# Kernel tuning notes

Measured on AMD Instinct MI355X. Metric: run time of the kernel, lower is better.

Reference implementation:

```python
import jax, jax.numpy as jnp
import numpy as np

N, E, G = 50000, 1600000, 500
H, F, NG, L, OUT = 128, 128, 50, 6, 1
LOG2 = float(np.log(2.0))

def ssp(x):
    return jax.nn.softplus(x) - LOG2

def setup_inputs() -> dict:
    key = jax.random.key(0)
    ks = jax.random.split(key, 16)
    inp = {
        'z': jax.random.randint(ks[0], (N,), 0, 100),
        'pos': jax.random.normal(ks[1], (N, 3), jnp.float32) * 5.0,
        'batch': jnp.sort(jax.random.randint(ks[2], (N,), 0, G)),
        'edge_index': jax.random.randint(ks[3], (2, E), 0, N),
        # parameters
        'emb': jax.random.normal(ks[4], (100, H), jnp.float32) * 0.1,
        'dist_W': jax.random.normal(ks[5], (1, NG), jnp.float32) * 0.1,
        'dist_b': jnp.zeros((NG,), jnp.float32),
        'Wn': jax.random.normal(ks[6], (L, H, F), jnp.float32) * (1.0 / np.sqrt(H)),
        'We': jax.random.normal(ks[7], (L, NG, F), jnp.float32) * (1.0 / np.sqrt(NG)),
        'be': jnp.zeros((L, F), jnp.float32),
        'Wo': jax.random.normal(ks[8], (L, F, H), jnp.float32) * (1.0 / np.sqrt(F)),
        'bo': jnp.zeros((L, H), jnp.float32),
        'W1': jax.random.normal(ks[9], (H, H // 2), jnp.float32) * (1.0 / np.sqrt(H)),
        'b1': jnp.zeros((H // 2,), jnp.float32),
        'W2': jax.random.normal(ks[10], (H // 2, OUT), jnp.float32) * (1.0 / np.sqrt(H // 2)),
        'b2': jnp.zeros((OUT,), jnp.float32),
    }
    return inp

def reference(z, pos, batch, edge_index, emb, dist_W, dist_b, Wn, We, be, Wo, bo, W1, b1, W2, b2):
    row, col = edge_index[0], edge_index[1]
    # edge distances -> Linear(1, num_gaussians)
    dist = jnp.linalg.norm(pos[row] - pos[col], axis=-1)            # [E]
    e = dist[:, None] * dist_W[0][None, :] + dist_b                 # [E, NG]
    v = emb[z]                                                      # [N, H]
    # edge-conditioned message passing x num_layers
    for i in range(Wn.shape[0]):
        h = v @ Wn[i]                                               # [N, F]
        msg = h[col] * (e @ We[i] + be[i])                          # [E, F]
        agg = jax.ops.segment_sum(msg, row, num_segments=v.shape[0])
        v = ssp(agg @ Wo[i] + bo[i])                                # [N, H]
    # readout
    u = ssp(v @ W1 + b1) @ W2 + b2                                  # [N, OUT]
    return jax.ops.segment_sum(u, batch, num_segments=G)            # [G, OUT]
```

## Files before the change

### kernel.cpp

```cpp
#include <hip/hip_runtime.h>
#include <math.h>

#define HDIM 128
#define NGAUSS 50
#define NLAYER 6
#define TSTR 136
#define DINV (1.0f/512.0f)
#define NXCD 8
#define NSTRIPE 512

typedef unsigned short ushortT;
typedef __attribute__((ext_vector_type(8))) short bf16x8;
typedef __attribute__((ext_vector_type(4))) float f32x4;

static __device__ __forceinline__ float bf2f(unsigned short u){
  union { unsigned int i; float f; } x; x.i = ((unsigned int)u) << 16; return x.f;
}
static __device__ __forceinline__ float bitsf(unsigned int i){
  union { unsigned int i; float f; } x; x.i = i; return x.f;
}
static __device__ __forceinline__ unsigned short f2bf(float f){
  union { float f; unsigned int i; } x; x.f = f;
  unsigned int i = x.i;
  unsigned int r = (i + 0x7FFFu + ((i >> 16) & 1u)) >> 16;
  return (unsigned short)r;
}
static __device__ __forceinline__ float ssp(float x){
  return fmaxf(x, 0.0f) + __logf(1.0f + __expf(-fabsf(x))) - 0.69314718055994530942f;
}
static __device__ __forceinline__ f32x4 mfma4r(const bf16x8* a, const bf16x8* b){
  f32x4 d = {0.f, 0.f, 0.f, 0.f};
  d = __builtin_amdgcn_mfma_f32_16x16x32_bf16(a[0], b[0], d, 0, 0, 0);
  d = __builtin_amdgcn_mfma_f32_16x16x32_bf16(a[1], b[1], d, 0, 0, 0);
  d = __builtin_amdgcn_mfma_f32_16x16x32_bf16(a[2], b[2], d, 0, 0, 0);
  d = __builtin_amdgcn_mfma_f32_16x16x32_bf16(a[3], b[3], d, 0, 0, 0);
  return d;
}


__global__ __launch_bounds__(256)
void k_colscan(int* __restrict__ hist, int* __restrict__ colTotal, int NB){
  __shared__ int sA[512], sB[512];
  int b = blockIdx.x, tid = threadIdx.x;
  sA[tid]       = hist[tid * 512 + b];
  sA[tid + 256] = hist[(tid + 256) * 512 + b];
  __syncthreads();
  int* pa = sA; int* pb = sB;
  for (int off = 1; off < 512; off <<= 1){
    for (int i = tid; i < 512; i += 256)
      pb[i] = pa[i] + (i >= off ? pa[i - off] : 0);
    __syncthreads();
    int* t = pa; pa = pb; pb = t;
  }
  int e0 = (tid == 0) ? 0 : pa[tid - 1];
  int e1 = pa[tid + 255];
  hist[tid * 512 + b]       = e0;
  hist[(tid + 256) * 512 + b] = e1;
  if (tid == 0) colTotal[b] = pa[511];
}

__global__ __launch_bounds__(256)
void k_bscan(const int* __restrict__ colTotal, int* __restrict__ bucketBase, int NB){
  __shared__ int sA[512], sB[512];
  int tid = threadIdx.x;
  for (int i = tid; i < 512; i += 256) sA[i] = (i < NB) ? colTotal[i] : 0;
  __syncthreads();
  int* pa = sA; int* pb = sB;
  for (int off = 1; off < 512; off <<= 1){
    for (int i = tid; i < 512; i += 256)
      pb[i] = pa[i] + (i >= off ? pa[i - off] : 0);
    __syncthreads();
    int* t = pa; pa = pb; pb = t;
  }
  for (int i = tid; i < NB; i += 256)
    bucketBase[i] = (i == 0) ? 0 : pa[i - 1];
  if (tid == 0) bucketBase[NB] = pa[NB - 1];
}

__global__ __launch_bounds__(256)
void k_scatter(const int* __restrict__ erow, const int* __restrict__ ecol,
               const float* __restrict__ pos, const int* __restrict__ hist,
               const int* __restrict__ bucketBase, uint2* __restrict__ stg,
               int E, int NB, int shift, int estripe){
  __shared__ int cur[512];
  int tid = threadIdx.x, w = blockIdx.x;
  for (int b = tid; b < NB; b += 256)
    cur[b] = bucketBase[b] + hist[w * 512 + b];
  __syncthreads();
  int beg = w * estripe;
  int end = beg + estripe; if (end > E) end = E;
  int mask = (1 << shift) - 1;
  for (int e = beg + tid; e < end; e += 256){
    int r = erow[e], c = ecol[e];
    float dx = pos[r*3+0] - pos[c*3+0];
    float dy = pos[r*3+1] - pos[c*3+1];
    float dz = pos[r*3+2] - pos[c*3+2];
    float d = sqrtf(dx*dx + dy*dy + dz*dz);
    int du = (int)(d * 512.0f + 0.5f);
    if (du > 65535) du = 65535;
    int p = atomicAdd(&cur[r >> shift], 1);
    uint2 t;
    t.x = ((unsigned int)c << 16) | (unsigned int)du;
    t.y = (unsigned int)(r & mask);
    stg[p] = t;
  }
}

__global__ __launch_bounds__(256)
void k_place(const uint2* __restrict__ stg, const int* __restrict__ bucketBase,
             int* __restrict__ offsets, unsigned int* __restrict__ csr,
             int N, int NB, int shift, int E){
  __shared__ int rc[1024];
  __shared__ int sA[1024], sB[1024];
  int b = blockIdx.x, tid = threadIdx.x;
  int R = 1 << shift;
  int r0 = b << shift;
  int s = bucketBase[b], e2 = bucketBase[b + 1];
  for (int i = tid; i < R; i += 256) rc[i] = 0;
  __syncthreads();
  for (int j = s + tid; j < e2; j += 256)
    atomicAdd(&rc[stg[j].y], 1);
  __syncthreads();
  for (int i = tid; i < R; i += 256) sA[i] = rc[i];
  __syncthreads();
  int* pa = sA; int* pb = sB;
  for (int off = 1; off < R; off <<= 1){
    for (int i = tid; i < R; i += 256)
      pb[i] = pa[i] + (i >= off ? pa[i - off] : 0);
    __syncthreads();
    int* t = pa; pa = pb; pb = t;
  }
  for (int i = tid; i < R; i += 256){
    int excl = (i == 0) ? 0 : pa[i - 1];
    rc[i] = excl;
    int r = r0 + i;
    if (r < N) offsets[r] = s + excl;
  }
  if (b == NB - 1 && tid == 0) offsets[N] = E;
  __syncthreads();
  for (int j = s + tid; j < e2; j += 256){
    uint2 t = stg[j];
    int slot = s + atomicAdd(&rc[t.y], 1);
    csr[slot] = t.x;
  }
}

__global__ __launch_bounds__(256)
void k_emb2(const float* __restrict__ emb, const float* __restrict__ Wn,
            ushortT* __restrict__ emb2){
  int idx = blockIdx.x * 256 + threadIdx.x;
  if (idx >= 100 * HDIM) return;
  int i = idx >> 7, f = idx & 127;
  float acc = 0.f;
  #pragma unroll 8
  for (int k = 0; k < HDIM; ++k)
    acc = fmaf(emb[i * HDIM + k], Wn[k * HDIM + f], acc);
  emb2[idx] = f2bf(acc);
}

__global__ void k_setup(const int* __restrict__ z, const ushortT* __restrict__ emb2,
                        ushortT* __restrict__ h0,
                        const float* __restrict__ Wn, ushortT* __restrict__ WnT,
                        const float* __restrict__ Wo, ushortT* __restrict__ WoT,
                        const float* __restrict__ dW, const float* __restrict__ db,
                        const float* __restrict__ We, const float* __restrict__ be,
                        float* __restrict__ a, float* __restrict__ c,
                        const int* __restrict__ batch, int* __restrict__ groupOff,
                        const float* __restrict__ W1, ushortT* __restrict__ W1T,
                        const int* __restrict__ erow, int* __restrict__ hist,
                        int N, int G, int E, int estripe, int NB, int shift,
                        int B1, int B2, int B4, int B5, int B7){
  __shared__ int lh[512];
  int b = blockIdx.x;
  int tid = threadIdx.x;
  if (b < B1){
    int base = (b * 256 + tid) * 8;
    if (base < N * HDIM){
      int n = base >> 7, f = base & 127;
      bf16x8 v = *(const bf16x8*)(emb2 + z[n] * HDIM + f);
      *(bf16x8*)(h0 + base) = v;
    }
    return;
  }
  b -= B1;
  if (b < B2){
    int base = (b * 256 + tid) * 8;
    if (base < NLAYER * HDIM * HDIM){
      int mat = base >> 14, rem = base & 16383;
      int n = rem >> 7, k0 = rem & 127;
      bf16x8 v;
      #pragma unroll
      for (int j = 0; j < 8; ++j)
        v[j] = (short)f2bf(Wn[(mat << 14) + (k0 + j) * HDIM + n]);
      *(bf16x8*)(WnT + base) = v;
    }
    return;
  }
  b -= B2;
  if (b < B2){
    int base = (b * 256 + tid) * 8;
    if (base < NLAYER * HDIM * HDIM){
      int mat = base >> 14, rem = base & 16383;
      int n = rem >> 7, k0 = rem & 127;
      bf16x8 v;
      #pragma unroll
      for (int j = 0; j < 8; ++j)
        v[j] = (short)f2bf(Wo[(mat << 14) + (k0 + j) * HDIM + n]);
      *(bf16x8*)(WoT + base) = v;
    }
    return;
  }
  b -= B2;
  if (b < B4){
    int idx = b * 256 + tid;
    if (idx < NLAYER * HDIM){
      int l = idx >> 7, f = idx & 127;
      float av = 0.f, cv = 0.f;
      for (int g = 0; g < NGAUSS; ++g){
        float we = We[(l * NGAUSS + g) * HDIM + f];
        av += dW[g] * we;
        cv += db[g] * we;
      }
      a[idx] = av;
      c[idx] = cv + be[idx];
    }
    return;
  }
  b -= B4;
  if (b < B5){
    int i = b * 256 + tid;
    if (i >= N) return;
    int bb = batch[i];
    if (i == 0){
      for (int g = 0; g <= bb; ++g) groupOff[g] = 0;
    } else {
      int pb = batch[i - 1];
      for (int g = pb + 1; g <= bb; ++g) groupOff[g] = i;
    }
    if (i == N - 1){
      for (int g = bb + 1; g <= G; ++g) groupOff[g] = N;
    }
    return;
  }
  b -= B5;
  if (b < B7){
    int base = (b * 256 + tid) * 8;
    if (base < 64 * HDIM){
      int ncol = base >> 7, k0 = base & 127;
      bf16x8 v;
      #pragma unroll
      for (int j = 0; j < 8; ++j)
        v[j] = (short)f2bf(W1[(k0 + j) * 64 + ncol]);
      *(bf16x8*)(W1T + base) = v;
    }
    return;
  }
  b -= B7;
  if (b < NSTRIPE){
    for (int i = tid; i < NB; i += 256) lh[i] = 0;
    __syncthreads();
    int beg = b * estripe;
    int end = beg + estripe; if (end > E) end = E;
    for (int e = beg + tid; e < end; e += 256)
      atomicAdd(&lh[erow[e] >> shift], 1);
    __syncthreads();
    for (int i = tid; i < NB; i += 256) hist[b * 512 + i] = lh[i];
  }
}

#define AGG_PROC(P, DD) do { \
    unsigned int w_; float lo_, hi_; \
    w_ = (P).x; lo_ = bitsf(w_ << 16); hi_ = bitsf(w_ & 0xFFFF0000u); \
    s1[0] = fmaf(lo_, (DD), s1[0]); s0[0] += lo_; \
    s1[1] = fmaf(hi_, (DD), s1[1]); s0[1] += hi_; \
    w_ = (P).y; lo_ = bitsf(w_ << 16); hi_ = bitsf(w_ & 0xFFFF0000u); \
    s1[2] = fmaf(lo_, (DD), s1[2]); s0[2] += lo_; \
    s1[3] = fmaf(hi_, (DD), s1[3]); s0[3] += hi_; \
    w_ = (P).z; lo_ = bitsf(w_ << 16); hi_ = bitsf(w_ & 0xFFFF0000u); \
    s1[4] = fmaf(lo_, (DD), s1[4]); s0[4] += lo_; \
    s1[5] = fmaf(hi_, (DD), s1[5]); s0[5] += hi_; \
    w_ = (P).w; lo_ = bitsf(w_ << 16); hi_ = bitsf(w_ & 0xFFFF0000u); \
    s1[6] = fmaf(lo_, (DD), s1[6]); s0[6] += lo_; \
    s1[7] = fmaf(hi_, (DD), s1[7]); s0[7] += hi_; \
  } while(0)

#define GATH(Q) (*(const uint4*)(h + ((size_t)((Q) >> 16) << 7) + fl))

__global__ __launch_bounds__(256, 6)
void k_agg2(const ushortT* __restrict__ h, const int* __restrict__ offsets,
            const unsigned int* __restrict__ cd, const float* __restrict__ a,
            const float* __restrict__ c, ushortT* __restrict__ aggHi,
            int N, int segNodes){
  int xcd = blockIdx.x & (NXCD - 1);
  int idx = blockIdx.x >> 3;
  int node = xcd * segNodes + idx * 4 + (threadIdx.x >> 6);
  if (node >= N || node >= (xcd + 1) * segNodes) return;
  int lane = threadIdx.x & 63;
  int quarter = lane >> 4;
  int fl = (lane & 15) * 8;
  int s = offsets[node], e = offsets[node + 1];
  float s0[8] = {0.f,0.f,0.f,0.f,0.f,0.f,0.f,0.f};
  float s1[8] = {0.f,0.f,0.f,0.f,0.f,0.f,0.f,0.f};
  int efull = s + ((e - s) & ~7);
  int L = s;
  if (efull - s >= 16){
    unsigned int qA0 = cd[L + quarter],      qA1 = cd[L + 4 + quarter];
    uint4 pA0 = GATH(qA0), pA1 = GATH(qA1);
    unsigned int qB0 = cd[L + 8 + quarter],  qB1 = cd[L + 12 + quarter];
    uint4 pB0 = GATH(qB0), pB1 = GATH(qB1);
    float dA0 = (float)(qA0 & 0xFFFFu) * DINV, dA1 = (float)(qA1 & 0xFFFFu) * DINV;
    float dB0 = (float)(qB0 & 0xFFFFu) * DINV, dB1 = (float)(qB1 & 0xFFFFu) * DINV;
    L += 16;
    for (; L + 16 <= efull; L += 16){
      unsigned int nA0 = cd[L + quarter], nA1 = cd[L + 4 + quarter];
      AGG_PROC(pA0, dA0); AGG_PROC(pA1, dA1);
      pA0 = GATH(nA0); pA1 = GATH(nA1);
      dA0 = (float)(nA0 & 0xFFFFu) * DINV; dA1 = (float)(nA1 & 0xFFFFu) * DINV;
      unsigned int nB0 = cd[L + 8 + quarter], nB1 = cd[L + 12 + quarter];
      AGG_PROC(pB0, dB0); AGG_PROC(pB1, dB1);
      pB0 = GATH(nB0); pB1 = GATH(nB1);
      dB0 = (float)(nB0 & 0xFFFFu) * DINV; dB1 = (float)(nB1 & 0xFFFFu) * DINV;
    }
    AGG_PROC(pA0, dA0); AGG_PROC(pA1, dA1);
    AGG_PROC(pB0, dB0); AGG_PROC(pB1, dB1);
  }
  for (; L + 8 <= efull; L += 8){
    unsigned int q0 = cd[L + quarter], q1 = cd[L + 4 + quarter];
    uint4 p0 = GATH(q0), p1 = GATH(q1);
    float d0 = (float)(q0 & 0xFFFFu) * DINV, d1 = (float)(q1 & 0xFFFFu) * DINV;
    AGG_PROC(p0, d0); AGG_PROC(p1, d1);
  }
  for (int j = efull; j < e; j += 4){
    int myj = j + quarter;
    if (myj < e){
      unsigned int q = cd[myj];
      uint4 p = GATH(q);
      float dd = (float)(q & 0xFFFFu) * DINV;
      AGG_PROC(p, dd);
    }
  }
  float4 av0 = *(const float4*)(a + fl);
  float4 av1 = *(const float4*)(a + fl + 4);
  float4 cv0 = *(const float4*)(c + fl);
  float4 cv1 = *(const float4*)(c + fl + 4);
  float r[8];
  r[0] = av0.x * s1[0] + cv0.x * s0[0];
  r[1] = av0.y * s1[1] + cv0.y * s0[1];
  r[2] = av0.z * s1[2] + cv0.z * s0[2];
  r[3] = av0.w * s1[3] + cv0.w * s0[3];
  r[4] = av1.x * s1[4] + cv1.x * s0[4];
  r[5] = av1.y * s1[5] + cv1.y * s0[5];
  r[6] = av1.z * s1[6] + cv1.z * s0[6];
  r[7] = av1.w * s1[7] + cv1.w * s0[7];
  #pragma unroll
  for (int k = 0; k < 8; ++k){
    r[k] += __shfl_down(r[k], 32, 64);
    r[k] += __shfl_down(r[k], 16, 64);
  }
  if (quarter == 0){
    uint4 st;
    st.x = (unsigned int)f2bf(r[0]) | ((unsigned int)f2bf(r[1]) << 16);
    st.y = (unsigned int)f2bf(r[2]) | ((unsigned int)f2bf(r[3]) << 16);
    st.z = (unsigned int)f2bf(r[4]) | ((unsigned int)f2bf(r[5]) << 16);
    st.w = (unsigned int)f2bf(r[6]) | ((unsigned int)f2bf(r[7]) << 16);
    *(uint4*)(aggHi + ((size_t)node << 7) + fl) = st;
  }
}

__global__ __launch_bounds__(256, 2)
void k_fpair(const ushortT* __restrict__ agg, const ushortT* __restrict__ WoT,
             const float* __restrict__ bo, const ushortT* __restrict__ WnT,
             ushortT* __restrict__ outH, int N, int segTiles){
  __shared__ ushortT vt[2][32 * TSTR];
  int tid = threadIdx.x;
  int wave = tid >> 6, lane = tid & 63;
  int pairI = wave >> 1, half = wave & 1;
  int m = lane & 15, quad = lane >> 4;
  int ntiles = (N + 15) >> 4;
  int xcd = blockIdx.x & (NXCD - 1);
  int idx = blockIdx.x >> 3;
  int wjIdx = idx * 2 + pairI;
  int segWJ = segTiles >> 1;
  int t0 = xcd * segTiles + wjIdx * 2;
  bool act = (wjIdx < segWJ) && (t0 < ntiles);
  ushortT* vw = vt[pairI];

  bf16x8 av[2][4];
  if (act){
    #pragma unroll
    for (int rt = 0; rt < 2; ++rt){
      int row = (t0 + rt) * 16 + m; if (row >= N) row = N - 1;
      #pragma unroll
      for (int kk = 0; kk < 4; ++kk)
        av[rt][kk] = *(const bf16x8*)(agg + ((size_t)row << 7) + kk*32 + quad*8);
    }
    #pragma unroll
    for (int cti = 0; cti < 4; ++cti){
      int ncol = (half * 4 + cti) * 16 + m;
      const ushortT* bp = WoT + ((size_t)ncol << 7) + quad*8;
      bf16x8 bb[4];
      #pragma unroll
      for (int kk = 0; kk < 4; ++kk) bb[kk] = *(const bf16x8*)(bp + kk*32);
      float bbias = bo[ncol];
      #pragma unroll
      for (int rt = 0; rt < 2; ++rt){
        f32x4 d = mfma4r(av[rt], bb);
        #pragma unroll
        for (int r = 0; r < 4; ++r)
          vw[(rt*16 + quad*4 + r) * TSTR + ncol] = f2bf(ssp(d[r] + bbias));
      }
    }
  }
  __syncthreads();
  if (act){
    bf16x8 a2[2][4];
    #pragma unroll
    for (int rt = 0; rt < 2; ++rt){
      #pragma unroll
      for (int kk = 0; kk < 4; ++kk)
        a2[rt][kk] = *(const bf16x8*)(&vw[(rt*16 + m) * TSTR + kk*32 + quad*8]);
    }
    #pragma unroll
    for (int cti = 0; cti < 4; ++cti){
      int ncol = (half * 4 + cti) * 16 + m;
      const ushortT* bp = WnT + ((size_t)ncol << 7) + quad*8;
      bf16x8 bb[4];
      #pragma unroll
      for (int kk = 0; kk < 4; ++kk) bb[kk] = *(const bf16x8*)(bp + kk*32);
      #pragma unroll
      for (int rt = 0; rt < 2; ++rt){
        f32x4 d = mfma4r(a2[rt], bb);
        #pragma unroll
        for (int r = 0; r < 4; ++r){
          int orow = (t0 + rt) * 16 + quad*4 + r;
          if (orow < N) outH[((size_t)orow << 7) + ncol] = f2bf(d[r]);
        }
      }
    }
  }
}

__global__ __launch_bounds__(256, 2)
void k_gfinal(const ushortT* __restrict__ agg, const ushortT* __restrict__ WoT,
              const float* __restrict__ bo, const ushortT* __restrict__ W1T,
              const float* __restrict__ b1, const float* __restrict__ W2,
              const float* __restrict__ b2, float* __restrict__ u,
              int N, int segTiles){
  __shared__ ushortT vt[2][32 * TSTR];
  __shared__ float part[2][2][32];
  int tid = threadIdx.x;
  int wave = tid >> 6, lane = tid & 63;
  int pairI = wave >> 1, half = wave & 1;
  int m = lane & 15, quad = lane >> 4;
  int ntiles = (N + 15) >> 4;
  int xcd = blockIdx.x & (NXCD - 1);
  int idx = blockIdx.x >> 3;
  int wjIdx = idx * 2 + pairI;
  int segWJ = segTiles >> 1;
  int t0 = xcd * segTiles + wjIdx * 2;
  bool act = (wjIdx < segWJ) && (t0 < ntiles);
  ushortT* vw = vt[pairI];

  if (act){
    bf16x8 av[2][4];
    #pragma unroll
    for (int rt = 0; rt < 2; ++rt){
      int row = (t0 + rt) * 16 + m; if (row >= N) row = N - 1;
      #pragma unroll
      for (int kk = 0; kk < 4; ++kk)
        av[rt][kk] = *(const bf16x8*)(agg + ((size_t)row << 7) + kk*32 + quad*8);
    }
    #pragma unroll
    for (int cti = 0; cti < 4; ++cti){
      int ncol = (half * 4 + cti) * 16 + m;
      const ushortT* bp = WoT + ((size_t)ncol << 7) + quad*8;
      bf16x8 bb[4];
      #pragma unroll
      for (int kk = 0; kk < 4; ++kk) bb[kk] = *(const bf16x8*)(bp + kk*32);
      float bbias = bo[ncol];
      #pragma unroll
      for (int rt = 0; rt < 2; ++rt){
        f32x4 d = mfma4r(av[rt], bb);
        #pragma unroll
        for (int r = 0; r < 4; ++r)
          vw[(rt*16 + quad*4 + r) * TSTR + ncol] = f2bf(ssp(d[r] + bbias));
      }
    }
  }
  __syncthreads();
  if (act){
    bf16x8 a2[2][4];
    #pragma unroll
    for (int rt = 0; rt < 2; ++rt){
      #pragma unroll
      for (int kk = 0; kk < 4; ++kk)
        a2[rt][kk] = *(const bf16x8*)(&vw[(rt*16 + m) * TSTR + kk*32 + quad*8]);
    }
    float acc[2][4] = {{0.f,0.f,0.f,0.f},{0.f,0.f,0.f,0.f}};
    #pragma unroll
    for (int cti = 0; cti < 2; ++cti){
      int ncol = (half * 2 + cti) * 16 + m;
      const ushortT* bp = W1T + ((size_t)ncol << 7) + quad*8;
      bf16x8 bb[4];
      #pragma unroll
      for (int kk = 0; kk < 4; ++kk) bb[kk] = *(const bf16x8*)(bp + kk*32);
      float bb1 = b1[ncol];
      float w2  = W2[ncol];
      #pragma unroll
      for (int rt = 0; rt < 2; ++rt){
        f32x4 d = mfma4r(a2[rt], bb);
        #pragma unroll
        for (int r = 0; r < 4; ++r)
          acc[rt][r] += ssp(d[r] + bb1) * w2;
      }
    }
    #pragma unroll
    for (int rt = 0; rt < 2; ++rt){
      #pragma unroll
      for (int r = 0; r < 4; ++r){
        float v = acc[rt][r];
        v += __shfl_xor(v, 1, 64);
        v += __shfl_xor(v, 2, 64);
        v += __shfl_xor(v, 4, 64);
        v += __shfl_xor(v, 8, 64);
        if (m == 0) part[pairI][half][rt*16 + quad*4 + r] = v;
      }
    }
  }
  __syncthreads();
  if (tid < 64){
    int p = tid >> 5, row = tid & 31;
    int wj = idx * 2 + p;
    int tt = xcd * segTiles + wj * 2;
    if (wj < segWJ && tt < ntiles){
      int orow = tt * 16 + row;
      if (orow < N) u[orow] = part[p][0][row] + part[p][1][row] + b2[0];
    }
  }
}

__global__ void k_gsum(const float* __restrict__ u, const int* __restrict__ groupOff,
                       float* __restrict__ out, int G){
  int g = blockIdx.x * 4 + (threadIdx.x >> 6);
  if (g >= G) return;
  int lane = threadIdx.x & 63;
  int s = groupOff[g], e = groupOff[g + 1];
  float acc = 0.f;
  for (int j = s + lane; j < e; j += 64) acc += u[j];
  #pragma unroll
  for (int off = 32; off > 0; off >>= 1)
    acc += __shfl_down(acc, off, 64);
  if (lane == 0) out[g] = acc;
}

extern "C" void kernel_launch(void* const* d_in, const int* in_sizes, int n_in,
                              void* d_out, int out_size, void* d_ws, size_t ws_size,
                              hipStream_t stream){
  const int N = in_sizes[0];
  const int E = in_sizes[3] / 2;
  const int G = out_size;

  const int*   z     = (const int*)d_in[0];
  const float* pos   = (const float*)d_in[1];
  const int*   batch = (const int*)d_in[2];
  const int*   eidx  = (const int*)d_in[3];
  const int*   erow  = eidx;
  const int*   ecol  = eidx + E;
  const float* emb   = (const float*)d_in[4];
  const float* dW    = (const float*)d_in[5];
  const float* db    = (const float*)d_in[6];
  const float* Wn    = (const float*)d_in[7];
  const float* We    = (const float*)d_in[8];
  const float* be    = (const float*)d_in[9];
  const float* Wo    = (const float*)d_in[10];
  const float* bo    = (const float*)d_in[11];
  const float* W1    = (const float*)d_in[12];
  const float* b1    = (const float*)d_in[13];
  const float* W2    = (const float*)d_in[14];
  const float* b2    = (const float*)d_in[15];

  char* ws = (char*)d_ws;
  size_t off = 0;
  auto alloc = [&](size_t bytes) -> char* {
    char* p = ws + off;
    off = (off + bytes + 255) & ~(size_t)255;
    return p;
  };
  size_t hbytes = (size_t)N * HDIM * 2;
  size_t stgbytes = (size_t)E * 8;
  int*          offsets  = (int*)         alloc((size_t)(N + 1) * 4);
  unsigned int* csr      = (unsigned int*)alloc((size_t)E * 4);
  ushortT*      h0       = (ushortT*)     alloc(hbytes);
  ushortT*      h1       = (ushortT*)     alloc(hbytes);
  ushortT*      agghi    = (ushortT*)     alloc(hbytes);
  ushortT*      stgbuf   = (ushortT*)     alloc(stgbytes);
  ushortT*      emb2     = (ushortT*)     alloc((size_t)100 * HDIM * 2);
  ushortT*      WnT      = (ushortT*)     alloc((size_t)NLAYER * HDIM * HDIM * 2);
  ushortT*      WoT      = (ushortT*)     alloc((size_t)NLAYER * HDIM * HDIM * 2);
  ushortT*      W1T      = (ushortT*)     alloc((size_t)64 * HDIM * 2);
  float*        a        = (float*)       alloc((size_t)NLAYER * HDIM * 4);
  float*        c        = (float*)       alloc((size_t)NLAYER * HDIM * 4);
  float*        u        = (float*)       alloc((size_t)N * 4);
  int*          groupOff = (int*)         alloc((size_t)(G + 1) * 4);

  int*   hist       = (int*)h1;
  int*   colTotal   = hist + NSTRIPE * 512;
  int*   bucketBase = colTotal + 512;
  uint2* stg        = (uint2*)stgbuf;

  int shift = 7;
  while ((((N - 1) >> shift) + 1) > 512) ++shift;
  int NB = ((N - 1) >> shift) + 1;
  int estripe = (E + NSTRIPE - 1) / NSTRIPE;

  int B1 = (N * HDIM / 8 + 255) / 256;
  int B2 = (NLAYER * HDIM * HDIM / 8 + 255) / 256;
  int B4 = (NLAYER * HDIM + 255) / 256;
  int B5 = (N + 255) / 256;
  int B7 = (64 * HDIM / 8 + 255) / 256;

  k_emb2<<<(100 * HDIM + 255) / 256, 256, 0, stream>>>(emb, Wn, emb2);
  k_setup<<<B1 + 2*B2 + B4 + B5 + B7 + NSTRIPE, 256, 0, stream>>>(
      z, emb2, h0, Wn, WnT, Wo, WoT,
      dW, db, We, be, a, c, batch, groupOff, W1, W1T,
      erow, hist,
      N, G, E, estripe, NB, shift, B1, B2, B4, B5, B7);

  k_colscan<<<NB,      256, 0, stream>>>(hist, colTotal, NB);
  k_bscan  <<<1,       256, 0, stream>>>(colTotal, bucketBase, NB);
  k_scatter<<<NSTRIPE, 256, 0, stream>>>(erow, ecol, pos, hist, bucketBase,
                                         stg, E, NB, shift, estripe);
  k_place  <<<NB,      256, 0, stream>>>(stg, bucketBase, offsets, csr, N, NB, shift, E);

  int ntiles = (N + 15) >> 4;
  int segTiles = (((ntiles + NXCD - 1) / NXCD) + 1) & ~1;
  int segNodes = segTiles * 16;
  int segWJ = segTiles >> 1;
  int aggGrid  = NXCD * ((segNodes + 3) / 4);
  int gGrid    = NXCD * ((segWJ + 1) / 2);

  for (int l = 0; l < NLAYER; ++l){
    size_t wo = (size_t)l * HDIM * HDIM;
    const ushortT* hin  = (l & 1) ? h1 : h0;
    ushortT*       hout = (l & 1) ? h0 : h1;
    k_agg2<<<aggGrid, 256, 0, stream>>>(hin, offsets, csr,
                                        a + l * HDIM, c + l * HDIM, agghi, N, segNodes);
    if (l < NLAYER - 1){
      size_t wn = (size_t)(l + 1) * HDIM * HDIM;
      k_fpair<<<gGrid, 256, 0, stream>>>(agghi, WoT + wo, bo + (size_t)l * HDIM,
                                         WnT + wn, hout, N, segTiles);
    } else {
      k_gfinal<<<gGrid, 256, 0, stream>>>(agghi, WoT + wo, bo + (size_t)l * HDIM,
                                          W1T, b1, W2, b2, u, N, segTiles);
    }
  }
  k_gsum<<<(G + 3) / 4, 256, 0, stream>>>(u, groupOff, (float*)d_out, G);
}
```

Before: 567.2 us.

## Fold small setup kernels into neighbours to cut launch count

Merges the embedding projection into the setup kernel and moves the h0 gather into the column-scan launch. The single-block bucket scan is dropped, and each scatter and place block recomputes the 512-entry scan itself. The group-sum kernel is replaced by atomic adds from the final readout kernel into an output that setup zeroes. This removes three kernel launches and the serialization they cause. In exchange each block does redundant scan work and there are float atomics on output, so summation order is no longer deterministic.

```diff
diff --git a/kernel.cpp b/kernel.cpp
--- a/kernel.cpp
+++ b/kernel.cpp
@@ -39,9 +39,19 @@
 
 
 __global__ __launch_bounds__(256)
-void k_colscan(int* __restrict__ hist, int* __restrict__ colTotal, int NB){
+void k_colscan(int* __restrict__ hist, int* __restrict__ colTotal,
+               const int* __restrict__ z, const ushortT* __restrict__ emb2,
+               ushortT* __restrict__ h0, int N, int NB){
   __shared__ int sA[512], sB[512];
   int b = blockIdx.x, tid = threadIdx.x;
+  if (b >= NB){
+    int base = ((b - NB) * 256 + tid) * 8;
+    if (base < N * HDIM){
+      int n = base >> 7, f = base & 127;
+      *(bf16x8*)(h0 + base) = *(const bf16x8*)(emb2 + z[n] * HDIM + f);
+    }
+    return;
+  }
   sA[tid]       = hist[tid * 512 + b];
   sA[tid + 256] = hist[(tid + 256) * 512 + b];
   __syncthreads();
@@ -60,9 +70,13 @@
 }
 
 __global__ __launch_bounds__(256)
-void k_bscan(const int* __restrict__ colTotal, int* __restrict__ bucketBase, int NB){
+void k_scatter(const int* __restrict__ erow, const int* __restrict__ ecol,
+               const float* __restrict__ pos, const int* __restrict__ hist,
+               const int* __restrict__ colTotal, uint2* __restrict__ stg,
+               int E, int NB, int shift, int estripe){
+  __shared__ int cur[512];
   __shared__ int sA[512], sB[512];
-  int tid = threadIdx.x;
+  int tid = threadIdx.x, w = blockIdx.x;
   for (int i = tid; i < 512; i += 256) sA[i] = (i < NB) ? colTotal[i] : 0;
   __syncthreads();
   int* pa = sA; int* pb = sB;
@@ -72,20 +86,8 @@
     __syncthreads();
     int* t = pa; pa = pb; pb = t;
   }
-  for (int i = tid; i < NB; i += 256)
-    bucketBase[i] = (i == 0) ? 0 : pa[i - 1];
-  if (tid == 0) bucketBase[NB] = pa[NB - 1];
-}
-
-__global__ __launch_bounds__(256)
-void k_scatter(const int* __restrict__ erow, const int* __restrict__ ecol,
-               const float* __restrict__ pos, const int* __restrict__ hist,
-               const int* __restrict__ bucketBase, uint2* __restrict__ stg,
-               int E, int NB, int shift, int estripe){
-  __shared__ int cur[512];
-  int tid = threadIdx.x, w = blockIdx.x;
   for (int b = tid; b < NB; b += 256)
-    cur[b] = bucketBase[b] + hist[w * 512 + b];
+    cur[b] = ((b == 0) ? 0 : pa[b - 1]) + hist[w * 512 + b];
   __syncthreads();
   int beg = w * estripe;
   int end = beg + estripe; if (end > E) end = E;
@@ -107,7 +109,7 @@
 }
 
 __global__ __launch_bounds__(256)
-void k_place(const uint2* __restrict__ stg, const int* __restrict__ bucketBase,
+void k_place(const uint2* __restrict__ stg, const int* __restrict__ colTotal,
              int* __restrict__ offsets, unsigned int* __restrict__ csr,
              int N, int NB, int shift, int E){
   __shared__ int rc[1024];
@@ -115,7 +117,18 @@
   int b = blockIdx.x, tid = threadIdx.x;
   int R = 1 << shift;
   int r0 = b << shift;
-  int s = bucketBase[b], e2 = bucketBase[b + 1];
+  for (int i = tid; i < 512; i += 256) sA[i] = (i < NB) ? colTotal[i] : 0;
+  __syncthreads();
+  int* pa = sA; int* pb = sB;
+  for (int off = 1; off < 512; off <<= 1){
+    for (int i = tid; i < 512; i += 256)
+      pb[i] = pa[i] + (i >= off ? pa[i - off] : 0);
+    __syncthreads();
+    int* t = pa; pa = pb; pb = t;
+  }
+  int s  = (b == 0) ? 0 : pa[b - 1];
+  int e2 = pa[b];
+  __syncthreads();
   for (int i = tid; i < R; i += 256) rc[i] = 0;
   __syncthreads();
   for (int j = s + tid; j < e2; j += 256)
@@ -123,7 +136,7 @@
   __syncthreads();
   for (int i = tid; i < R; i += 256) sA[i] = rc[i];
   __syncthreads();
-  int* pa = sA; int* pb = sB;
+  pa = sA; pb = sB;
   for (int off = 1; off < R; off <<= 1){
     for (int i = tid; i < R; i += 256)
       pb[i] = pa[i] + (i >= off ? pa[i - off] : 0);
@@ -145,44 +158,34 @@
   }
 }
 
-__global__ __launch_bounds__(256)
-void k_emb2(const float* __restrict__ emb, const float* __restrict__ Wn,
-            ushortT* __restrict__ emb2){
-  int idx = blockIdx.x * 256 + threadIdx.x;
-  if (idx >= 100 * HDIM) return;
-  int i = idx >> 7, f = idx & 127;
-  float acc = 0.f;
-  #pragma unroll 8
-  for (int k = 0; k < HDIM; ++k)
-    acc = fmaf(emb[i * HDIM + k], Wn[k * HDIM + f], acc);
-  emb2[idx] = f2bf(acc);
-}
-
-__global__ void k_setup(const int* __restrict__ z, const ushortT* __restrict__ emb2,
-                        ushortT* __restrict__ h0,
+__global__ void k_setup(const float* __restrict__ emb,
+                        ushortT* __restrict__ emb2,
                         const float* __restrict__ Wn, ushortT* __restrict__ WnT,
                         const float* __restrict__ Wo, ushortT* __restrict__ WoT,
                         const float* __restrict__ dW, const float* __restrict__ db,
                         const float* __restrict__ We, const float* __restrict__ be,
                         float* __restrict__ a, float* __restrict__ c,
-                        const int* __restrict__ batch, int* __restrict__ groupOff,
                         const float* __restrict__ W1, ushortT* __restrict__ W1T,
                         const int* __restrict__ erow, int* __restrict__ hist,
+                        float* __restrict__ outz,
                         int N, int G, int E, int estripe, int NB, int shift,
-                        int B1, int B2, int B4, int B5, int B7){
+                        int B0, int B2, int B4, int B7){
   __shared__ int lh[512];
   int b = blockIdx.x;
   int tid = threadIdx.x;
-  if (b < B1){
-    int base = (b * 256 + tid) * 8;
-    if (base < N * HDIM){
-      int n = base >> 7, f = base & 127;
-      bf16x8 v = *(const bf16x8*)(emb2 + z[n] * HDIM + f);
-      *(bf16x8*)(h0 + base) = v;
+  if (b < B0){
+    int idx = b * 256 + tid;
+    if (idx < 100 * HDIM){
+      int i = idx >> 7, f = idx & 127;
+      float acc = 0.f;
+      #pragma unroll 8
+      for (int k = 0; k < HDIM; ++k)
+        acc = fmaf(emb[i * HDIM + k], Wn[k * HDIM + f], acc);
+      emb2[idx] = f2bf(acc);
     }
     return;
   }
-  b -= B1;
+  b -= B0;
   if (b < B2){
     int base = (b * 256 + tid) * 8;
     if (base < NLAYER * HDIM * HDIM){
@@ -224,25 +227,10 @@
       a[idx] = av;
       c[idx] = cv + be[idx];
     }
+    for (int g = b * 256 + tid; g < G; g += B4 * 256) outz[g] = 0.f;
     return;
   }
   b -= B4;
-  if (b < B5){
-    int i = b * 256 + tid;
-    if (i >= N) return;
-    int bb = batch[i];
-    if (i == 0){
-      for (int g = 0; g <= bb; ++g) groupOff[g] = 0;
-    } else {
-      int pb = batch[i - 1];
-      for (int g = pb + 1; g <= bb; ++g) groupOff[g] = i;
-    }
-    if (i == N - 1){
-      for (int g = bb + 1; g <= G; ++g) groupOff[g] = N;
-    }
-    return;
-  }
-  b -= B5;
   if (b < B7){
     int base = (b * 256 + tid) * 8;
     if (base < 64 * HDIM){
@@ -444,8 +432,8 @@
 void k_gfinal(const ushortT* __restrict__ agg, const ushortT* __restrict__ WoT,
               const float* __restrict__ bo, const ushortT* __restrict__ W1T,
               const float* __restrict__ b1, const float* __restrict__ W2,
-              const float* __restrict__ b2, float* __restrict__ u,
-              int N, int segTiles){
+              const float* __restrict__ b2, const int* __restrict__ batch,
+              float* __restrict__ out, int N, int segTiles){
   __shared__ ushortT vt[2][32 * TSTR];
   __shared__ float part[2][2][32];
   int tid = threadIdx.x;
@@ -534,23 +522,12 @@
     int tt = xcd * segTiles + wj * 2;
     if (wj < segWJ && tt < ntiles){
       int orow = tt * 16 + row;
-      if (orow < N) u[orow] = part[p][0][row] + part[p][1][row] + b2[0];
-    }
-  }
-}
-
-__global__ void k_gsum(const float* __restrict__ u, const int* __restrict__ groupOff,
-                       float* __restrict__ out, int G){
-  int g = blockIdx.x * 4 + (threadIdx.x >> 6);
-  if (g >= G) return;
-  int lane = threadIdx.x & 63;
-  int s = groupOff[g], e = groupOff[g + 1];
-  float acc = 0.f;
-  for (int j = s + lane; j < e; j += 64) acc += u[j];
-  #pragma unroll
-  for (int off = 32; off > 0; off >>= 1)
-    acc += __shfl_down(acc, off, 64);
-  if (lane == 0) out[g] = acc;
+      if (orow < N){
+        float v = part[p][0][row] + part[p][1][row] + b2[0];
+        atomicAdd(&out[batch[orow]], v);
+      }
+    }
+  }
 }
 
 extern "C" void kernel_launch(void* const* d_in, const int* in_sizes, int n_in,
@@ -600,12 +577,9 @@
   ushortT*      W1T      = (ushortT*)     alloc((size_t)64 * HDIM * 2);
   float*        a        = (float*)       alloc((size_t)NLAYER * HDIM * 4);
   float*        c        = (float*)       alloc((size_t)NLAYER * HDIM * 4);
-  float*        u        = (float*)       alloc((size_t)N * 4);
-  int*          groupOff = (int*)         alloc((size_t)(G + 1) * 4);
 
   int*   hist       = (int*)h1;
   int*   colTotal   = hist + NSTRIPE * 512;
-  int*   bucketBase = colTotal + 512;
   uint2* stg        = (uint2*)stgbuf;
 
   int shift = 7;
@@ -613,24 +587,22 @@
   int NB = ((N - 1) >> shift) + 1;
   int estripe = (E + NSTRIPE - 1) / NSTRIPE;
 
-  int B1 = (N * HDIM / 8 + 255) / 256;
+  int B0 = (100 * HDIM + 255) / 256;
   int B2 = (NLAYER * HDIM * HDIM / 8 + 255) / 256;
   int B4 = (NLAYER * HDIM + 255) / 256;
-  int B5 = (N + 255) / 256;
   int B7 = (64 * HDIM / 8 + 255) / 256;
-
-  k_emb2<<<(100 * HDIM + 255) / 256, 256, 0, stream>>>(emb, Wn, emb2);
-  k_setup<<<B1 + 2*B2 + B4 + B5 + B7 + NSTRIPE, 256, 0, stream>>>(
-      z, emb2, h0, Wn, WnT, Wo, WoT,
-      dW, db, We, be, a, c, batch, groupOff, W1, W1T,
-      erow, hist,
-      N, G, E, estripe, NB, shift, B1, B2, B4, B5, B7);
-
-  k_colscan<<<NB,      256, 0, stream>>>(hist, colTotal, NB);
-  k_bscan  <<<1,       256, 0, stream>>>(colTotal, bucketBase, NB);
-  k_scatter<<<NSTRIPE, 256, 0, stream>>>(erow, ecol, pos, hist, bucketBase,
+  int B1h = (N * HDIM / 8 + 255) / 256;
+
+  k_setup<<<B0 + 2*B2 + B4 + B7 + NSTRIPE, 256, 0, stream>>>(
+      emb, emb2, Wn, WnT, Wo, WoT,
+      dW, db, We, be, a, c, W1, W1T,
+      erow, hist, (float*)d_out,
+      N, G, E, estripe, NB, shift, B0, B2, B4, B7);
+
+  k_colscan<<<NB + B1h, 256, 0, stream>>>(hist, colTotal, z, emb2, h0, N, NB);
+  k_scatter<<<NSTRIPE, 256, 0, stream>>>(erow, ecol, pos, hist, colTotal,
                                          stg, E, NB, shift, estripe);
-  k_place  <<<NB,      256, 0, stream>>>(stg, bucketBase, offsets, csr, N, NB, shift, E);
+  k_place  <<<NB,      256, 0, stream>>>(stg, colTotal, offsets, csr, N, NB, shift, E);
 
   int ntiles = (N + 15) >> 4;
   int segTiles = (((ntiles + NXCD - 1) / NXCD) + 1) & ~1;
@@ -651,8 +623,8 @@
                                          WnT + wn, hout, N, segTiles);
     } else {
       k_gfinal<<<gGrid, 256, 0, stream>>>(agghi, WoT + wo, bo + (size_t)l * HDIM,
-                                          W1T, b1, W2, b2, u, N, segTiles);
-    }
-  }
-  k_gsum<<<(G + 3) / 4, 256, 0, stream>>>(u, groupOff, (float*)d_out, G);
-}
+                                          W1T, b1, W2, b2, batch,
+                                          (float*)d_out, N, segTiles);
+    }
+  }
+}
```

Measured after the change: 592.8 us. 1.05x slower.
